# Kernel optimization log

Measured on AMD Instinct MI355X. Metric: run time of the kernel, lower is better.

Reference implementation:

```python
import jax, jax.numpy as jnp
import numpy as np

N_LEVELS = 16  # 2**4, bit = 4 in QuantLinear


def _sum_to(g, shape):
    # reduce grad g to broadcast shape `shape`
    extra = g.ndim - len(shape)
    if extra:
        g = g.sum(axis=tuple(range(extra)))
    axes = tuple(i for i, (gs, s) in enumerate(zip(g.shape, shape)) if s == 1 and gs != 1)
    if axes:
        g = g.sum(axis=axes, keepdims=True)
    return g.reshape(shape)


@jax.custom_vjp
def ste_round(x):
    return jnp.round(x)

def _r_fwd(x):
    return jnp.round(x), None

def _r_bwd(_, g):
    return (g,)

ste_round.defvjp(_r_fwd, _r_bwd)


@jax.custom_vjp
def dclip(x, lo, hi):
    return jnp.clip(x, lo, hi)

def _c_fwd(x, lo, hi):
    return jnp.clip(x, lo, hi), (x, lo, hi)

def _c_bwd(res, g):
    x, lo, hi = res
    gx = jnp.where((x < lo) | (x > hi), 0.0, g)
    glo = _sum_to(jnp.where(x > lo, 0.0, g), lo.shape)
    ghi = _sum_to(jnp.where(x < hi, 0.0, g), hi.shape)
    return gx, glo, ghi

dclip.defvjp(_c_fwd, _c_bwd)


def fake_quant(x, lb, ub):
    # UniformQuantizer.forward
    delta = (ub - lb) / (N_LEVELS - 1)
    x_cut = dclip(x, lb, ub)
    x_int = ste_round((x_cut - lb) / delta)
    return x_int * delta + lb


def setup_inputs() -> dict:
    key = jax.random.key(0)
    k0, k1, k2 = jax.random.split(key, 3)
    B, S, Din, Dout = 4, 4096, 1024, 3072
    x = jax.random.normal(k0, (B, S, Din), jnp.float32)
    weight = jax.random.normal(k1, (Dout, Din), jnp.float32) * 0.02
    bias = jax.random.normal(k2, (Dout,), jnp.float32) * 0.01
    # calibrated per-tensor activation bounds, per-output-channel weight bounds
    in_lb = jnp.full((1,), -2.5, jnp.float32)
    in_ub = jnp.full((1,), 2.5, jnp.float32)
    w_ub = jnp.max(jnp.abs(weight), axis=1, keepdims=True)  # (Dout, 1)
    w_lb = -w_ub
    return {"x": x, "weight": weight, "bias": bias,
            "in_lb": in_lb, "in_ub": in_ub, "w_lb": w_lb, "w_ub": w_ub}


def reference(x, weight, bias, in_lb, in_ub, w_lb, w_ub):
    qx = fake_quant(x, in_lb, in_ub)        # [B,S,Din]
    qw = fake_quant(weight, w_lb, w_ub)     # [Dout,Din]
    return jnp.einsum('bsi,oi->bso', qx, qw) + bias
```

## Files before the change

kernel.cpp:

```cpp
#include <hip/hip_runtime.h>

typedef int i32x4 __attribute__((ext_vector_type(4)));
typedef unsigned char u8x8 __attribute__((ext_vector_type(8)));


__global__ __launch_bounds__(512) void quant_x_i8(
    const float* __restrict__ x, unsigned char* __restrict__ qx,
    float* __restrict__ Sx, const float* __restrict__ lbp,
    const float* __restrict__ ubp) {
  const float lb = lbp[0], ub = ubp[0];
  const float delta = (ub - lb) / 15.0f;
  const int tid = threadIdx.x;
  const int row_in_blk = tid >> 7;
  const int row = blockIdx.x * 4 + row_in_blk;
  const size_t base = (size_t)row * 1024 + (tid & 127) * 8;

  const float4* p = reinterpret_cast<const float4*>(x + base);
  float4 v0 = p[0], v1 = p[1];
  int k[8];
  float vv[8] = {v0.x, v0.y, v0.z, v0.w, v1.x, v1.y, v1.z, v1.w};
  int s = 0;
  u8x8 o;
#pragma unroll
  for (int j = 0; j < 8; ++j) {
    float t = fminf(fmaxf(vv[j], lb), ub);
    k[j] = (int)rintf((t - lb) / delta);
    s += k[j];
    o[j] = (unsigned char)k[j];
  }
  *reinterpret_cast<u8x8*>(qx + base) = o;

#pragma unroll
  for (int d = 32; d > 0; d >>= 1) s += __shfl_down(s, d);
  __shared__ int wsum[8];
  if ((tid & 63) == 0) wsum[tid >> 6] = s;
  __syncthreads();
  if (tid < 4) Sx[blockIdx.x * 4 + tid] = (float)(wsum[2 * tid] + wsum[2 * tid + 1]);
}

__global__ __launch_bounds__(512) void quant_w_i8(
    const float* __restrict__ w, unsigned char* __restrict__ qw,
    float* __restrict__ Sw, const float* __restrict__ lbp,
    const float* __restrict__ ubp) {
  const int tid = threadIdx.x;
  const int row_in_blk = tid >> 7;
  const int row = blockIdx.x * 4 + row_in_blk;
  const float lb = lbp[row], ub = ubp[row];
  const float delta = (ub - lb) / 15.0f;
  const size_t base = (size_t)row * 1024 + (tid & 127) * 8;

  const float4* p = reinterpret_cast<const float4*>(w + base);
  float4 v0 = p[0], v1 = p[1];
  float vv[8] = {v0.x, v0.y, v0.z, v0.w, v1.x, v1.y, v1.z, v1.w};
  int s = 0;
  u8x8 o;
#pragma unroll
  for (int j = 0; j < 8; ++j) {
    float t = fminf(fmaxf(vv[j], lb), ub);
    int k = (int)rintf((t - lb) / delta);
    s += k;
    o[j] = (unsigned char)k;
  }
  *reinterpret_cast<u8x8*>(qw + base) = o;

#pragma unroll
  for (int d = 32; d > 0; d >>= 1) s += __shfl_down(s, d);
  __shared__ int wsum[8];
  if ((tid & 63) == 0) wsum[tid >> 6] = s;
  __syncthreads();
  if (tid < 4) Sw[blockIdx.x * 4 + tid] = (float)(wsum[2 * tid] + wsum[2 * tid + 1]);
}


__device__ __forceinline__ void gload_lds16(const unsigned char* g, unsigned char* l) {
  __builtin_amdgcn_global_load_lds(
      (const __attribute__((address_space(1))) unsigned int*)g,
      (__attribute__((address_space(3))) unsigned int*)l, 16, 0, 0);
}

#define SWZ(o) ((o) ^ ((((o) >> 7) & 3) << 4))

__global__ __launch_bounds__(512, 4) void gemm_i8_kernel(
    const unsigned char* __restrict__ A, const unsigned char* __restrict__ B,
    const float* __restrict__ bias, const float* __restrict__ Sx,
    const float* __restrict__ Sw, const float* __restrict__ wlb,
    const float* __restrict__ wub, const float* __restrict__ xlb,
    const float* __restrict__ xub, float* __restrict__ C, int M, int N) {
  const int K = 1024;
  const int NKT = 16;
  __shared__ unsigned char lds[3][24576];

  const int tid = threadIdx.x;
  const int w = tid >> 6, l = tid & 63;
  const int wm = w >> 1, wn = w & 1;

  int bid = blockIdx.x;
  { const int cpx = gridDim.x >> 3; bid = (bid & 7) * cpx + (bid >> 3); }
  const int ntn = N >> 7;
  const int tm = bid / ntn, tn = bid % ntn;

  const unsigned char* gA = A + (size_t)tm * 256 * K;
  const unsigned char* gB = B + (size_t)tn * 128 * K;

  const int p0 = tid * 16, p1 = 8192 + tid * 16, pB = tid * 16;
  const int o0 = SWZ(p0), o1 = SWZ(p1), oB = SWZ(pB);
  const unsigned char* sA0 = gA + (size_t)(o0 >> 6) * K + (o0 & 63);
  const unsigned char* sA1 = gA + (size_t)(o1 >> 6) * K + (o1 & 63);
  const unsigned char* sB0 = gB + (size_t)(oB >> 6) * K + (oB & 63);

  const int lroff = (l & 15) * 64 + (((l >> 4) * 16) ^ (((l >> 1) & 3) << 4));

#define STAGE(SB, KOFF) do {                                             \
    unsigned char* Rb_ = &lds[SB][0];                                    \
    gload_lds16(sA0 + (KOFF), Rb_ + p0);                                 \
    gload_lds16(sA1 + (KOFF), Rb_ + p1);                                 \
    gload_lds16(sB0 + (KOFF), Rb_ + 16384 + pB);                         \
  } while (0)

#define RD_A(RB, F)  (*(const i32x4*)(&lds[RB][0]     + wm * 4096 + (F) * 1024 + lroff))
#define RD_B(RB, NN) (*(const i32x4*)(&lds[RB][16384] + wn * 4096 + (NN) * 1024 + lroff))

#define BAR __builtin_amdgcn_s_barrier()
#define LGKM0 do { asm volatile("s_waitcnt lgkmcnt(0)" ::: "memory");    \
                   __builtin_amdgcn_sched_barrier(0); } while (0)
#define VMC3 asm volatile("s_waitcnt vmcnt(3)" ::: "memory")

  i32x4 acc[4][4] = {};
  i32x4 av[4], bv[4];

  STAGE(0, 0);
  STAGE(1, 64);
  VMC3; BAR;

#pragma unroll
  for (int t = 0; t < NKT; ++t) {
    const int rb = t % 3, sb = (t + 2) % 3;
    const int koff = (t + 2 < NKT ? (t + 2) : 0) << 6;
#pragma unroll
    for (int f = 0; f < 4; ++f) av[f] = RD_A(rb, f);
#pragma unroll
    for (int nn = 0; nn < 4; ++nn) bv[nn] = RD_B(rb, nn);
    STAGE(sb, koff);
    VMC3;
    BAR; LGKM0;
    __builtin_amdgcn_s_setprio(1);
#pragma unroll
    for (int mm = 0; mm < 4; ++mm)
#pragma unroll
      for (int nn = 0; nn < 4; ++nn)
        acc[mm][nn] = __builtin_amdgcn_mfma_i32_16x16x64_i8(
            av[mm], bv[nn], acc[mm][nn], 0, 0, 0);
    __builtin_amdgcn_s_setprio(0);
    BAR;
  }

  const float lbx = xlb[0];
  const float dx = (xub[0] - lbx) / 15.0f;
  const int rq = (l >> 4) * 4;
  const int cn = l & 15;
  const int mb = tm * 256 + wm * 64;
  const int nb = tn * 128 + wn * 64;

  float sxr[4][4];
#pragma unroll
  for (int m = 0; m < 4; ++m) {
    const int r0 = mb + m * 16 + rq;
#pragma unroll
    for (int j = 0; j < 4; ++j) sxr[m][j] = Sx[r0 + j];
  }
#pragma unroll
  for (int n = 0; n < 4; ++n) {
    const int col = nb + n * 16 + cn;
    const float wl = wlb[col], wu = wub[col];
    const float dw = (wu - wl) / 15.0f;
    const float c1 = dx * dw;
    const float c2 = dx * wl;
    const float c3 = lbx * dw * Sw[col] + 1024.0f * lbx * wl + bias[col];
#pragma unroll
    for (int m = 0; m < 4; ++m) {
      float* cp = C + (size_t)(mb + m * 16 + rq) * N + col;
      cp[0]             = c1 * (float)acc[m][n][0] + c2 * sxr[m][0] + c3;
      cp[(size_t)N]     = c1 * (float)acc[m][n][1] + c2 * sxr[m][1] + c3;
      cp[(size_t)2 * N] = c1 * (float)acc[m][n][2] + c2 * sxr[m][2] + c3;
      cp[(size_t)3 * N] = c1 * (float)acc[m][n][3] + c2 * sxr[m][3] + c3;
    }
  }
#undef STAGE
#undef RD_A
#undef RD_B
#undef BAR
#undef LGKM0
#undef VMC3
}

extern "C" void kernel_launch(void* const* d_in, const int* in_sizes, int n_in,
                              void* d_out, int out_size, void* d_ws, size_t ws_size,
                              hipStream_t stream) {
  const float* x     = (const float*)d_in[0];
  const float* wgt   = (const float*)d_in[1];
  const float* bias  = (const float*)d_in[2];
  const float* in_lb = (const float*)d_in[3];
  const float* in_ub = (const float*)d_in[4];
  const float* w_lb  = (const float*)d_in[5];
  const float* w_ub  = (const float*)d_in[6];

  const int Dout = in_sizes[2];
  const int Din  = in_sizes[1] / Dout;
  const int M    = in_sizes[0] / Din;

  unsigned char* qx = (unsigned char*)d_ws;
  unsigned char* qw = qx + (size_t)M * Din;
  float* Sx = (float*)(qw + (size_t)Dout * Din);
  float* Sw = Sx + M;

  quant_x_i8<<<M / 4, 512, 0, stream>>>(x, qx, Sx, in_lb, in_ub);
  quant_w_i8<<<Dout / 4, 512, 0, stream>>>(wgt, qw, Sw, w_lb, w_ub);

  dim3 grid((M / 256) * (Dout / 128));
  gemm_i8_kernel<<<grid, 512, 0, stream>>>(qx, qw, bias, Sx, Sw, w_lb, w_ub,
                                           in_lb, in_ub, (float*)d_out, M, Dout);
}
```

Measured before the change: 99.31 us.

## Fuse quant kernels, split GEMM K-step into two MFMA halves, nontemporal stores

```diff
diff --git a/kernel.cpp b/kernel.cpp
--- a/kernel.cpp
+++ b/kernel.cpp
@@ -4,52 +4,28 @@
 typedef unsigned char u8x8 __attribute__((ext_vector_type(8)));
 
 
-__global__ __launch_bounds__(512) void quant_x_i8(
+__global__ __launch_bounds__(512) void quant_i8_fused(
     const float* __restrict__ x, unsigned char* __restrict__ qx,
-    float* __restrict__ Sx, const float* __restrict__ lbp,
-    const float* __restrict__ ubp) {
-  const float lb = lbp[0], ub = ubp[0];
+    float* __restrict__ Sx, const float* __restrict__ xlb,
+    const float* __restrict__ xub, const float* __restrict__ w,
+    unsigned char* __restrict__ qw, float* __restrict__ Sw,
+    const float* __restrict__ wlb, const float* __restrict__ wub,
+    int nxblocks) {
+  const int tid = threadIdx.x;
+  const int rloc = tid >> 7;
+  const bool is_x = (int)blockIdx.x < nxblocks;
+  const int rb = is_x ? blockIdx.x : blockIdx.x - nxblocks;
+  const int row = rb * 4 + rloc;
+
+  const float* src = is_x ? x : w;
+  unsigned char* dst = is_x ? qx : qw;
+  float* Sdst = is_x ? Sx : Sw;
+  const float lb = is_x ? xlb[0] : wlb[row];
+  const float ub = is_x ? xub[0] : wub[row];
   const float delta = (ub - lb) / 15.0f;
-  const int tid = threadIdx.x;
-  const int row_in_blk = tid >> 7;
-  const int row = blockIdx.x * 4 + row_in_blk;
+
   const size_t base = (size_t)row * 1024 + (tid & 127) * 8;
-
-  const float4* p = reinterpret_cast<const float4*>(x + base);
-  float4 v0 = p[0], v1 = p[1];
-  int k[8];
-  float vv[8] = {v0.x, v0.y, v0.z, v0.w, v1.x, v1.y, v1.z, v1.w};
-  int s = 0;
-  u8x8 o;
-#pragma unroll
-  for (int j = 0; j < 8; ++j) {
-    float t = fminf(fmaxf(vv[j], lb), ub);
-    k[j] = (int)rintf((t - lb) / delta);
-    s += k[j];
-    o[j] = (unsigned char)k[j];
-  }
-  *reinterpret_cast<u8x8*>(qx + base) = o;
-
-#pragma unroll
-  for (int d = 32; d > 0; d >>= 1) s += __shfl_down(s, d);
-  __shared__ int wsum[8];
-  if ((tid & 63) == 0) wsum[tid >> 6] = s;
-  __syncthreads();
-  if (tid < 4) Sx[blockIdx.x * 4 + tid] = (float)(wsum[2 * tid] + wsum[2 * tid + 1]);
-}
-
-__global__ __launch_bounds__(512) void quant_w_i8(
-    const float* __restrict__ w, unsigned char* __restrict__ qw,
-    float* __restrict__ Sw, const float* __restrict__ lbp,
-    const float* __restrict__ ubp) {
-  const int tid = threadIdx.x;
-  const int row_in_blk = tid >> 7;
-  const int row = blockIdx.x * 4 + row_in_blk;
-  const float lb = lbp[row], ub = ubp[row];
-  const float delta = (ub - lb) / 15.0f;
-  const size_t base = (size_t)row * 1024 + (tid & 127) * 8;
-
-  const float4* p = reinterpret_cast<const float4*>(w + base);
+  const float4* p = reinterpret_cast<const float4*>(src + base);
   float4 v0 = p[0], v1 = p[1];
   float vv[8] = {v0.x, v0.y, v0.z, v0.w, v1.x, v1.y, v1.z, v1.w};
   int s = 0;
@@ -61,14 +37,14 @@
     s += k;
     o[j] = (unsigned char)k;
   }
-  *reinterpret_cast<u8x8*>(qw + base) = o;
+  *reinterpret_cast<u8x8*>(dst + base) = o;
 
 #pragma unroll
   for (int d = 32; d > 0; d >>= 1) s += __shfl_down(s, d);
   __shared__ int wsum[8];
   if ((tid & 63) == 0) wsum[tid >> 6] = s;
   __syncthreads();
-  if (tid < 4) Sw[blockIdx.x * 4 + tid] = (float)(wsum[2 * tid] + wsum[2 * tid + 1]);
+  if (tid < 4) Sdst[rb * 4 + tid] = (float)(wsum[2 * tid] + wsum[2 * tid + 1]);
 }
 
 
@@ -80,7 +56,7 @@
 
 #define SWZ(o) ((o) ^ ((((o) >> 7) & 3) << 4))
 
-__global__ __launch_bounds__(512, 4) void gemm_i8_kernel(
+__global__ __launch_bounds__(512, 2) void gemm_i8_kernel(
     const unsigned char* __restrict__ A, const unsigned char* __restrict__ B,
     const float* __restrict__ bias, const float* __restrict__ Sx,
     const float* __restrict__ Sw, const float* __restrict__ wlb,
@@ -110,11 +86,13 @@
 
   const int lroff = (l & 15) * 64 + (((l >> 4) * 16) ^ (((l >> 1) & 3) << 4));
 
-#define STAGE(SB, KOFF) do {                                             \
+#define STAGE_A(SB, KOFF) do {                                           \
     unsigned char* Rb_ = &lds[SB][0];                                    \
     gload_lds16(sA0 + (KOFF), Rb_ + p0);                                 \
     gload_lds16(sA1 + (KOFF), Rb_ + p1);                                 \
-    gload_lds16(sB0 + (KOFF), Rb_ + 16384 + pB);                         \
+  } while (0)
+#define STAGE_B(SB, KOFF) do {                                           \
+    gload_lds16(sB0 + (KOFF), &lds[SB][16384] + pB);                     \
   } while (0)
 
 #define RD_A(RB, F)  (*(const i32x4*)(&lds[RB][0]     + wm * 4096 + (F) * 1024 + lroff))
@@ -126,31 +104,39 @@
 #define VMC3 asm volatile("s_waitcnt vmcnt(3)" ::: "memory")
 
   i32x4 acc[4][4] = {};
-  i32x4 av[4], bv[4];
-
-  STAGE(0, 0);
-  STAGE(1, 64);
+  i32x4 av0, av1, av2, av3, bv[4];
+
+#define MFMA_HALF(A0, A1, MH) do {                                       \
+    __builtin_amdgcn_s_setprio(1);                                       \
+    _Pragma("unroll") for (int nn = 0; nn < 4; ++nn)                     \
+      acc[(MH) * 2 + 0][nn] = __builtin_amdgcn_mfma_i32_16x16x64_i8(     \
+          A0, bv[nn], acc[(MH) * 2 + 0][nn], 0, 0, 0);                   \
+    _Pragma("unroll") for (int nn = 0; nn < 4; ++nn)                     \
+      acc[(MH) * 2 + 1][nn] = __builtin_amdgcn_mfma_i32_16x16x64_i8(     \
+          A1, bv[nn], acc[(MH) * 2 + 1][nn], 0, 0, 0);                   \
+    __builtin_amdgcn_s_setprio(0);                                       \
+  } while (0)
+
+  STAGE_A(0, 0); STAGE_B(0, 0);
+  STAGE_A(1, 64); STAGE_B(1, 64);
   VMC3; BAR;
 
 #pragma unroll
   for (int t = 0; t < NKT; ++t) {
     const int rb = t % 3, sb = (t + 2) % 3;
     const int koff = (t + 2 < NKT ? (t + 2) : 0) << 6;
-#pragma unroll
-    for (int f = 0; f < 4; ++f) av[f] = RD_A(rb, f);
+    av0 = RD_A(rb, 0); av1 = RD_A(rb, 1);
 #pragma unroll
     for (int nn = 0; nn < 4; ++nn) bv[nn] = RD_B(rb, nn);
-    STAGE(sb, koff);
+    STAGE_A(sb, koff);
+    BAR; LGKM0;
+    MFMA_HALF(av0, av1, 0);
+    BAR;
+    av2 = RD_A(rb, 2); av3 = RD_A(rb, 3);
+    STAGE_B(sb, koff);
     VMC3;
     BAR; LGKM0;
-    __builtin_amdgcn_s_setprio(1);
-#pragma unroll
-    for (int mm = 0; mm < 4; ++mm)
-#pragma unroll
-      for (int nn = 0; nn < 4; ++nn)
-        acc[mm][nn] = __builtin_amdgcn_mfma_i32_16x16x64_i8(
-            av[mm], bv[nn], acc[mm][nn], 0, 0, 0);
-    __builtin_amdgcn_s_setprio(0);
+    MFMA_HALF(av2, av3, 1);
     BAR;
   }
 
@@ -179,18 +165,21 @@
 #pragma unroll
     for (int m = 0; m < 4; ++m) {
       float* cp = C + (size_t)(mb + m * 16 + rq) * N + col;
-      cp[0]             = c1 * (float)acc[m][n][0] + c2 * sxr[m][0] + c3;
-      cp[(size_t)N]     = c1 * (float)acc[m][n][1] + c2 * sxr[m][1] + c3;
-      cp[(size_t)2 * N] = c1 * (float)acc[m][n][2] + c2 * sxr[m][2] + c3;
-      cp[(size_t)3 * N] = c1 * (float)acc[m][n][3] + c2 * sxr[m][3] + c3;
+      __builtin_nontemporal_store(c1 * (float)acc[m][n][0] + c2 * sxr[m][0] + c3, cp);
+      __builtin_nontemporal_store(c1 * (float)acc[m][n][1] + c2 * sxr[m][1] + c3, cp + (size_t)N);
+      __builtin_nontemporal_store(c1 * (float)acc[m][n][2] + c2 * sxr[m][2] + c3, cp + (size_t)2 * N);
+      __builtin_nontemporal_store(c1 * (float)acc[m][n][3] + c2 * sxr[m][3] + c3, cp + (size_t)3 * N);
     }
   }
-#undef STAGE
+  asm volatile("s_waitcnt vmcnt(0)" ::: "memory");
+#undef STAGE_A
+#undef STAGE_B
 #undef RD_A
 #undef RD_B
 #undef BAR
 #undef LGKM0
 #undef VMC3
+#undef MFMA_HALF
 }
 
 extern "C" void kernel_launch(void* const* d_in, const int* in_sizes, int n_in,
@@ -213,8 +202,9 @@
   float* Sx = (float*)(qw + (size_t)Dout * Din);
   float* Sw = Sx + M;
 
-  quant_x_i8<<<M / 4, 512, 0, stream>>>(x, qx, Sx, in_lb, in_ub);
-  quant_w_i8<<<Dout / 4, 512, 0, stream>>>(wgt, qw, Sw, w_lb, w_ub);
+  const int nxb = M / 4;
+  quant_i8_fused<<<nxb + Dout / 4, 512, 0, stream>>>(
+      x, qx, Sx, in_lb, in_ub, wgt, qw, Sw, w_lb, w_ub, nxb);
 
   dim3 grid((M / 256) * (Dout / 128));
   gemm_i8_kernel<<<grid, 512, 0, stream>>>(qx, qw, bias, Sx, Sw, w_lb, w_ub,
```

After: 94.66 us (median of 2 runs). 1.05x faster.
